# Kernel optimization log

Measured on AMD Instinct MI355X. Metric: run time of the kernel, lower is better.

The kernel has to match this reference:

```python
import jax, jax.numpy as jnp
import numpy as np

V, E, H, L = 100000, 128, 512, 9
B, T = 64, 512


def setup_inputs() -> dict:
    key = jax.random.key(0)
    ks = jax.random.split(key, 8)
    text = jax.random.randint(ks[0], (B, T), 0, V, dtype=jnp.int32)
    labels = jax.random.randint(ks[1], (B, T), 0, L, dtype=jnp.int32)
    embed = jax.random.normal(ks[2], (V, E), jnp.float32) * 0.02
    Wx = jax.random.normal(ks[3], (E, 4 * H), jnp.float32) * (1.0 / np.sqrt(E))
    Wh = jax.random.normal(ks[4], (H, 4 * H), jnp.float32) * (1.0 / np.sqrt(H))
    # Keras LSTM default: zero bias with unit forget-gate bias (gate order i,f,c,o)
    b = jnp.zeros((4 * H,), jnp.float32).at[H:2 * H].set(1.0)
    Wd = jax.random.normal(ks[5], (H, L), jnp.float32) * (1.0 / np.sqrt(H))
    bd = jnp.zeros((L,), jnp.float32)
    trans = jax.random.uniform(ks[6], (L, L), jnp.float32)
    return dict(text=text, labels=labels, embed=embed, Wx=Wx, Wh=Wh, b=b,
                Wd=Wd, bd=bd, trans=trans)


def _lstm(x, Wx, Wh, b):
    # x: [B,T,E] -> h: [B,T,H]; Keras gate order i,f,c,o
    Bx, Tx, _ = x.shape
    Hh = Wh.shape[0]
    xg = jnp.einsum('bte,eg->btg', x, Wx) + b  # precompute input projections [B,T,4H]

    def step(carry, g_t):
        h, c = carry
        g = g_t + h @ Wh
        i, f, cg, o = jnp.split(g, 4, axis=-1)
        c = jax.nn.sigmoid(f) * c + jax.nn.sigmoid(i) * jnp.tanh(cg)
        h = jax.nn.sigmoid(o) * jnp.tanh(c)
        return (h, c), h

    init = (jnp.zeros((Bx, Hh), x.dtype), jnp.zeros((Bx, Hh), x.dtype))
    _, hs = jax.lax.scan(step, init, jnp.moveaxis(xg, 1, 0))
    return jnp.moveaxis(hs, 0, 1)


def _crf_log_likelihood(logits, labels, lens, trans):
    # tfa.text.crf_log_likelihood: score(seq) - log_norm (forward algorithm)
    Bl, Tl, Ll = logits.shape
    t_idx = jnp.arange(Tl)
    mask = t_idx[None, :] < lens[:, None]  # [B,T]
    unary = jnp.take_along_axis(logits, labels[..., None], axis=2)[..., 0]
    unary = jnp.where(mask, unary, 0.0).sum(-1)
    binary = trans[labels[:, :-1], labels[:, 1:]]
    bmask = t_idx[1:][None, :] < lens[:, None]  # transition t->t+1 counts iff t+1 < len
    binary = jnp.where(bmask, binary, 0.0).sum(-1)
    score = unary + binary

    def step(alpha, xs):
        lg, t = xs  # lg: [B,L]
        new = jax.scipy.special.logsumexp(alpha[:, :, None] + trans[None], axis=1) + lg
        alpha = jnp.where((t < lens)[:, None], new, alpha)
        return alpha, None

    alpha0 = logits[:, 0]
    xs = (jnp.moveaxis(logits[:, 1:], 1, 0), jnp.arange(1, Tl))
    alpha, _ = jax.lax.scan(step, alpha0, xs)
    log_norm = jax.scipy.special.logsumexp(alpha, axis=-1)
    return score - log_norm


def reference(text, labels, embed, Wx, Wh, b, Wd, bd, trans):
    lens = jnp.sum((text != 0).astype(jnp.int32), axis=-1)
    x = embed[text]                      # [B,T,E] (dropout inactive at inference)
    h = _lstm(x, Wx, Wh, b)              # [B,T,H]
    logits = h @ Wd + bd                 # [B,T,L]
    ll = _crf_log_likelihood(logits, labels, lens, trans)  # [B]
    return logits, lens, ll
```

## Files before the change

kernel.cpp:

```cpp
#include <hip/hip_runtime.h>
#include <hip/hip_bf16.h>

#define V_SZ 100000
#define E_SZ 128
#define H_SZ 512
#define L_SZ 9
#define B_SZ 64
#define T_SZ 512
#define G4   (4*H_SZ)

#define LOGITS_N (B_SZ*T_SZ*L_SZ)
#define HS_BYTES ((size_t)B_SZ*T_SZ*H_SZ*2)

typedef short bf16x8 __attribute__((ext_vector_type(8)));
typedef float f32x4  __attribute__((ext_vector_type(4)));

static __device__ __forceinline__ unsigned short f2bf(float x){
  unsigned int u = __builtin_bit_cast(unsigned int, x);
  unsigned int r = (u + 0x7fffu + ((u >> 16) & 1u)) >> 16;
  return (unsigned short)r;
}
static __device__ __forceinline__ float bf2f(unsigned short b){
  unsigned int u = ((unsigned int)b) << 16;
  return __builtin_bit_cast(float, u);
}
static __device__ __forceinline__ float sig_f(float x){
  return 1.f / (1.f + __expf(-x));
}
static __device__ __forceinline__ float tanh_f(float x){
  float a = fabsf(x);
  float e = __expf(-2.f * a);
  float t = (1.f - e) / (1.f + e);
  return copysignf(t, x);
}

__global__ void k_lens(const int* __restrict__ text, float* __restrict__ out_lens){
  int b = blockIdx.x;
  int c = 0;
  for (int t = threadIdx.x; t < T_SZ; t += 256)
    c += (text[b*T_SZ + t] != 0);
  for (int off = 32; off; off >>= 1) c += __shfl_down(c, off, 64);
  __shared__ int sred[4];
  int w = threadIdx.x >> 6;
  if ((threadIdx.x & 63) == 0) sred[w] = c;
  __syncthreads();
  if (threadIdx.x == 0)
    out_lens[b] = (float)(sred[0] + sred[1] + sred[2] + sred[3]);
}

__global__ __launch_bounds__(256, 1)
void k_lstm(const int* __restrict__ text, const float* __restrict__ embed,
            const float* __restrict__ Wx, const float* __restrict__ Wh,
            const float* __restrict__ bias, unsigned short* __restrict__ hs,
            int* __restrict__ flags)
{
  const int g    = blockIdx.x & 7;
  const int j    = blockIdx.x >> 3;
  const int n0   = j * 16;
  const int tid  = threadIdx.x;
  const int w    = tid >> 6;
  const int lane = tid & 63;
  const int q    = lane >> 4;
  const int l16  = lane & 15;

  __shared__ unsigned short h_lds[16*512];
  __shared__ unsigned short x_lds[16*128];
  __shared__ float gate_lds[4][8][16];

  for (int i = tid; i < 16*512; i += 256) h_lds[i] = 0;
  for (int i = tid; i < 16*128; i += 256) x_lds[i] = 0;

  const int gcol = w * H_SZ + n0 + l16;
  bf16x8 Whf[16];
#pragma unroll
  for (int kk = 0; kk < 16; ++kk){
    bf16x8 v;
#pragma unroll
    for (int jj = 0; jj < 8; ++jj)
      v[jj] = (short)f2bf(Wh[(long)(kk*32 + q*8 + jj)*G4 + gcol]);
    Whf[kk] = v;
  }
  bf16x8 Wxf[4];
#pragma unroll
  for (int kk = 0; kk < 4; ++kk){
    bf16x8 v;
#pragma unroll
    for (int jj = 0; jj < 8; ++jj)
      v[jj] = (short)f2bf(Wx[(long)(kk*32 + q*8 + jj)*G4 + gcol]);
    Wxf[kk] = v;
  }
  const float biasv = bias[gcol];

  float cs0 = 0.f, cs1 = 0.f;
  const int gr = tid >> 3;
  const int gc2 = (tid & 7) * 2;

  __syncthreads();

  for (int t = 0; t < T_SZ; ++t){
    {
      int xr = tid >> 5;
      int c4 = (tid & 31) * 4;
      int idx = text[(g*8 + xr)*T_SZ + t];
      const float4 xv = *(const float4*)(embed + (long)idx*E_SZ + c4);
      int cb = c4 * 2;
      unsigned short* p = (unsigned short*)((char*)x_lds + xr*256 + (cb ^ (xr << 4)));
      p[0] = f2bf(xv.x); p[1] = f2bf(xv.y); p[2] = f2bf(xv.z); p[3] = f2bf(xv.w);
    }

    if (t > 0){
      if (tid < 64){
        const int* fl = flags + (g*T_SZ + (t-1))*32;
        int it = 0;
        for (;;){
          int f = 1;
          if (lane < 32)
            f = __hip_atomic_load(&fl[lane], __ATOMIC_RELAXED, __HIP_MEMORY_SCOPE_AGENT);
          if (__all(f != 0)) break;
          if (++it > (1 << 20)) break;
        }
      }
      __syncthreads();

#pragma unroll
      for (int c = 0; c < 4; ++c){
        int chunk = tid + 256*c;
        int hr    = chunk >> 7;
        int k4    = chunk & 127;
        unsigned long long v = __hip_atomic_load(
            (const unsigned long long*)(hs + ((long)(g*8 + hr)*T_SZ + (t-1))*H_SZ + k4*4),
            __ATOMIC_RELAXED, __HIP_MEMORY_SCOPE_AGENT);
        int cb = k4 * 8;
        *(unsigned long long*)((char*)h_lds + hr*1024 + (cb ^ (hr << 4))) = v;
      }
    }
    __syncthreads();

    f32x4 acc0 = {0.f,0.f,0.f,0.f}, acc1 = {0.f,0.f,0.f,0.f};
#pragma unroll
    for (int kk = 0; kk < 4; ++kk){
      bf16x8 a = *(const bf16x8*)((const char*)x_lds + l16*256 + ((kk*64 + q*16) ^ (l16 << 4)));
      if (kk & 1) acc1 = __builtin_amdgcn_mfma_f32_16x16x32_bf16(a, Wxf[kk], acc1, 0, 0, 0);
      else        acc0 = __builtin_amdgcn_mfma_f32_16x16x32_bf16(a, Wxf[kk], acc0, 0, 0, 0);
    }
    if (t > 0){
#pragma unroll
      for (int kk = 0; kk < 16; ++kk){
        bf16x8 a = *(const bf16x8*)((const char*)h_lds + l16*1024 + ((kk*64 + q*16) ^ (l16 << 4)));
        if (kk & 1) acc1 = __builtin_amdgcn_mfma_f32_16x16x32_bf16(a, Whf[kk], acc1, 0, 0, 0);
        else        acc0 = __builtin_amdgcn_mfma_f32_16x16x32_bf16(a, Whf[kk], acc0, 0, 0, 0);
      }
    }
#pragma unroll
    for (int rg = 0; rg < 4; ++rg){
      int row = q*4 + rg;
      if (row < 8) gate_lds[w][row][l16] = acc0[rg] + acc1[rg] + biasv;
    }
    __syncthreads();

    if (tid < 64){
      float gi0 = gate_lds[0][gr][gc2],   gi1 = gate_lds[0][gr][gc2+1];
      float gf0 = gate_lds[1][gr][gc2],   gf1 = gate_lds[1][gr][gc2+1];
      float gg0 = gate_lds[2][gr][gc2],   gg1 = gate_lds[2][gr][gc2+1];
      float go0 = gate_lds[3][gr][gc2],   go1 = gate_lds[3][gr][gc2+1];
      cs0 = sig_f(gf0)*cs0 + sig_f(gi0)*tanh_f(gg0);
      cs1 = sig_f(gf1)*cs1 + sig_f(gi1)*tanh_f(gg1);
      float h0 = sig_f(go0)*tanh_f(cs0);
      float h1 = sig_f(go1)*tanh_f(cs1);
      unsigned int pk = (unsigned int)f2bf(h0) | ((unsigned int)f2bf(h1) << 16);
      __hip_atomic_store(
          (unsigned int*)(hs + ((long)(g*8 + gr)*T_SZ + t)*H_SZ + n0 + gc2), pk,
          __ATOMIC_RELAXED, __HIP_MEMORY_SCOPE_AGENT);
      asm volatile("s_waitcnt vmcnt(0)" ::: "memory");
      if (tid == 0)
        __hip_atomic_store(&flags[(g*T_SZ + t)*32 + j], 1,
                           __ATOMIC_RELAXED, __HIP_MEMORY_SCOPE_AGENT);
    }
  }
}

__global__ void k_logits(const unsigned short* __restrict__ hs,
                         const float* __restrict__ Wd, const float* __restrict__ bd,
                         float* __restrict__ out)
{
  __shared__ float wd_s[H_SZ*L_SZ];
  __shared__ float bd_s[L_SZ];
  for (int i = threadIdx.x; i < H_SZ*L_SZ; i += 128) wd_s[i] = Wd[i];
  if (threadIdx.x < L_SZ) bd_s[threadIdx.x] = bd[threadIdx.x];
  __syncthreads();

  long row = (long)blockIdx.x*128 + threadIdx.x;
  const unsigned short* hp = hs + row*H_SZ;
  float acc[9];
#pragma unroll
  for (int jj = 0; jj < 9; ++jj) acc[jj] = 0.f;
  for (int k = 0; k < H_SZ; k += 8){
    uint4 v = *(const uint4*)(hp + k);
    const unsigned short* u = (const unsigned short*)&v;
#pragma unroll
    for (int l = 0; l < 8; ++l){
      float hf = bf2f(u[l]);
#pragma unroll
      for (int jj = 0; jj < 9; ++jj)
        acc[jj] = fmaf(hf, wd_s[(k + l)*L_SZ + jj], acc[jj]);
    }
  }
  float* op = out + row*L_SZ;
#pragma unroll
  for (int jj = 0; jj < 9; ++jj) op[jj] = acc[jj] + bd_s[jj];
}

__global__ void k_crf(const float* __restrict__ logits, const int* __restrict__ labels,
                      const float* __restrict__ trans, const float* __restrict__ lensf,
                      float* __restrict__ out_ll)
{
  int b = blockIdx.x;
  int lane = threadIdx.x;
  int len = (int)lensf[b];
  const float* lg  = logits + (long)b*T_SZ*L_SZ;
  const int*   lab = labels + b*T_SZ;

  float s = 0.f;
  for (int t = lane; t < T_SZ; t += 64){
    if (t < len){
      s += lg[t*L_SZ + lab[t]];
      if (t >= 1) s += trans[lab[t-1]*L_SZ + lab[t]];
    }
  }
  for (int off = 32; off; off >>= 1) s += __shfl_down(s, off, 64);

  float tr[9];
#pragma unroll
  for (int i = 0; i < 9; ++i) tr[i] = (lane < 9) ? trans[i*L_SZ + lane] : 0.f;
  float alpha = (lane < 9) ? lg[lane] : -1e30f;

  for (int t = 1; t < T_SZ; ++t){
    float tmp[9];
    float m = -1e30f;
#pragma unroll
    for (int i = 0; i < 9; ++i){
      float ai = __shfl(alpha, i, 64);
      tmp[i] = ai + tr[i];
      m = fmaxf(m, tmp[i]);
    }
    float e = 0.f;
#pragma unroll
    for (int i = 0; i < 9; ++i) e += __expf(tmp[i] - m);
    float lgv = (lane < 9) ? lg[t*L_SZ + lane] : 0.f;
    float nv = m + __logf(e) + lgv;
    if (t < len && lane < 9) alpha = nv;
  }

  float mm = (lane < 9) ? alpha : -1e30f;
  for (int off = 8; off; off >>= 1) mm = fmaxf(mm, __shfl_down(mm, off, 64));
  mm = __shfl(mm, 0, 64);
  float ee = (lane < 9) ? __expf(alpha - mm) : 0.f;
  for (int off = 8; off; off >>= 1) ee += __shfl_down(ee, off, 64);
  if (lane == 0) out_ll[b] = s - (mm + __logf(ee));
}

extern "C" void kernel_launch(void* const* d_in, const int* in_sizes, int n_in,
                              void* d_out, int out_size, void* d_ws, size_t ws_size,
                              hipStream_t stream)
{
  const int*   text   = (const int*)  d_in[0];
  const int*   labels = (const int*)  d_in[1];
  const float* embed  = (const float*)d_in[2];
  const float* Wx     = (const float*)d_in[3];
  const float* Wh     = (const float*)d_in[4];
  const float* bias   = (const float*)d_in[5];
  const float* Wd     = (const float*)d_in[6];
  const float* bd     = (const float*)d_in[7];
  const float* trans  = (const float*)d_in[8];

  float* out        = (float*)d_out;
  float* out_logits = out;
  float* out_lens   = out + LOGITS_N;
  float* out_ll     = out + LOGITS_N + B_SZ;

  unsigned short* hs = (unsigned short*)d_ws;
  int* flags = (int*)((char*)d_ws + HS_BYTES);

  hipMemsetAsync(flags, 0, 8*T_SZ*32*sizeof(int), stream);
  k_lens  <<<B_SZ, 256, 0, stream>>>(text, out_lens);
  k_lstm  <<<256, 256, 0, stream>>>(text, embed, Wx, Wh, bias, hs, flags);
  k_logits<<<256, 128, 0, stream>>>(hs, Wd, bd, out_logits);
  k_crf   <<<B_SZ, 64, 0, stream>>>(out_logits, labels, trans, out_lens, out_ll);
}
```

Measured before the change: 1.731 ms.

## Replace flag-based LSTM sync with sentinel polling and interleave two batch groups per block

The hidden-state buffer is pre-filled with a NaN sentinel so consumer blocks poll the h data directly instead of separate per-step flags. This removes the flag writes, the vmcnt wait and one barrier from each step. Each block now handles two batch groups in alternation, halving the grid to 128 blocks so one group's latency can hide behind the other's work. It adds a full 32MB sentinel reset pass, and a real bf16 value equal to the sentinel pattern would cause a spin until timeout. The CRF max reduction is also restructured into a tree.

```diff
diff --git a/kernel.cpp b/kernel.cpp
--- a/kernel.cpp
+++ b/kernel.cpp
@@ -11,6 +11,8 @@
 
 #define LOGITS_N (B_SZ*T_SZ*L_SZ)
 #define HS_BYTES ((size_t)B_SZ*T_SZ*H_SZ*2)
+#define SENT32 0x7FC07FC0u
+#define SENT64 0x7FC07FC07FC07FC0ull
 
 typedef short bf16x8 __attribute__((ext_vector_type(8)));
 typedef float f32x4  __attribute__((ext_vector_type(4)));
@@ -32,6 +34,12 @@
   float e = __expf(-2.f * a);
   float t = (1.f - e) / (1.f + e);
   return copysignf(t, x);
+}
+
+__global__ void k_reset(unsigned long long* __restrict__ hs64){
+  const long n = HS_BYTES / 8;
+  for (long i = (long)blockIdx.x*256 + threadIdx.x; i < n; i += (long)gridDim.x*256)
+    __hip_atomic_store(&hs64[i], SENT64, __ATOMIC_RELAXED, __HIP_MEMORY_SCOPE_AGENT);
 }
 
 __global__ void k_lens(const int* __restrict__ text, float* __restrict__ out_lens){
@@ -51,11 +59,11 @@
 __global__ __launch_bounds__(256, 1)
 void k_lstm(const int* __restrict__ text, const float* __restrict__ embed,
             const float* __restrict__ Wx, const float* __restrict__ Wh,
-            const float* __restrict__ bias, unsigned short* __restrict__ hs,
-            int* __restrict__ flags)
+            const float* __restrict__ bias, unsigned short* __restrict__ hs)
 {
-  const int g    = blockIdx.x & 7;
-  const int j    = blockIdx.x >> 3;
+  const int p    = blockIdx.x & 3;
+  const int j    = blockIdx.x >> 2;
+  const int gA   = 2*p, gB = 2*p + 1;
   const int n0   = j * 16;
   const int tid  = threadIdx.x;
   const int w    = tid >> 6;
@@ -91,47 +99,48 @@
   }
   const float biasv = bias[gcol];
 
-  float cs0 = 0.f, cs1 = 0.f;
-  const int gr = tid >> 3;
+  float csA0 = 0.f, csA1 = 0.f, csB0 = 0.f, csB1 = 0.f;
+  const int gr  = tid >> 3;
   const int gc2 = (tid & 7) * 2;
 
+  const int k4     = tid & 127;
+  const int hrbase = tid >> 7;
+
   __syncthreads();
 
-  for (int t = 0; t < T_SZ; ++t){
+  auto phase = [&](int g, int t, float& cs0, float& cs1){
     {
       int xr = tid >> 5;
       int c4 = (tid & 31) * 4;
       int idx = text[(g*8 + xr)*T_SZ + t];
       const float4 xv = *(const float4*)(embed + (long)idx*E_SZ + c4);
       int cb = c4 * 2;
-      unsigned short* p = (unsigned short*)((char*)x_lds + xr*256 + (cb ^ (xr << 4)));
-      p[0] = f2bf(xv.x); p[1] = f2bf(xv.y); p[2] = f2bf(xv.z); p[3] = f2bf(xv.w);
+      unsigned short* pp = (unsigned short*)((char*)x_lds + xr*256 + (cb ^ (xr << 4)));
+      pp[0] = f2bf(xv.x); pp[1] = f2bf(xv.y); pp[2] = f2bf(xv.z); pp[3] = f2bf(xv.w);
     }
 
     if (t > 0){
-      if (tid < 64){
-        const int* fl = flags + (g*T_SZ + (t-1))*32;
-        int it = 0;
-        for (;;){
-          int f = 1;
-          if (lane < 32)
-            f = __hip_atomic_load(&fl[lane], __ATOMIC_RELAXED, __HIP_MEMORY_SCOPE_AGENT);
-          if (__all(f != 0)) break;
-          if (++it > (1 << 20)) break;
+      unsigned long long v[4];
+      int it = 0; bool ok;
+      do {
+        ok = true;
+#pragma unroll
+        for (int c = 0; c < 4; ++c){
+          int hrow = hrbase + 2*c;
+          v[c] = __hip_atomic_load(
+              (const unsigned long long*)(hs + ((long)(g*8 + hrow)*T_SZ + (t-1))*H_SZ + k4*4),
+              __ATOMIC_RELAXED, __HIP_MEMORY_SCOPE_AGENT);
         }
-      }
-      __syncthreads();
-
+#pragma unroll
+        for (int c = 0; c < 4; ++c){
+          unsigned int lo = (unsigned int)v[c], hi = (unsigned int)(v[c] >> 32);
+          ok = ok && (lo != SENT32) && (hi != SENT32);
+        }
+      } while (!ok && ++it < (1 << 20));
 #pragma unroll
       for (int c = 0; c < 4; ++c){
-        int chunk = tid + 256*c;
-        int hr    = chunk >> 7;
-        int k4    = chunk & 127;
-        unsigned long long v = __hip_atomic_load(
-            (const unsigned long long*)(hs + ((long)(g*8 + hr)*T_SZ + (t-1))*H_SZ + k4*4),
-            __ATOMIC_RELAXED, __HIP_MEMORY_SCOPE_AGENT);
-        int cb = k4 * 8;
-        *(unsigned long long*)((char*)h_lds + hr*1024 + (cb ^ (hr << 4))) = v;
+        int hrow = hrbase + 2*c;
+        *(unsigned long long*)((char*)h_lds + hrow*1024 + ((k4*8) ^ (hrow << 4))) = v[c];
       }
     }
     __syncthreads();
@@ -159,10 +168,10 @@
     __syncthreads();
 
     if (tid < 64){
-      float gi0 = gate_lds[0][gr][gc2],   gi1 = gate_lds[0][gr][gc2+1];
-      float gf0 = gate_lds[1][gr][gc2],   gf1 = gate_lds[1][gr][gc2+1];
-      float gg0 = gate_lds[2][gr][gc2],   gg1 = gate_lds[2][gr][gc2+1];
-      float go0 = gate_lds[3][gr][gc2],   go1 = gate_lds[3][gr][gc2+1];
+      float gi0 = gate_lds[0][gr][gc2], gi1 = gate_lds[0][gr][gc2+1];
+      float gf0 = gate_lds[1][gr][gc2], gf1 = gate_lds[1][gr][gc2+1];
+      float gg0 = gate_lds[2][gr][gc2], gg1 = gate_lds[2][gr][gc2+1];
+      float go0 = gate_lds[3][gr][gc2], go1 = gate_lds[3][gr][gc2+1];
       cs0 = sig_f(gf0)*cs0 + sig_f(gi0)*tanh_f(gg0);
       cs1 = sig_f(gf1)*cs1 + sig_f(gi1)*tanh_f(gg1);
       float h0 = sig_f(go0)*tanh_f(cs0);
@@ -171,11 +180,12 @@
       __hip_atomic_store(
           (unsigned int*)(hs + ((long)(g*8 + gr)*T_SZ + t)*H_SZ + n0 + gc2), pk,
           __ATOMIC_RELAXED, __HIP_MEMORY_SCOPE_AGENT);
-      asm volatile("s_waitcnt vmcnt(0)" ::: "memory");
-      if (tid == 0)
-        __hip_atomic_store(&flags[(g*T_SZ + t)*32 + j], 1,
-                           __ATOMIC_RELAXED, __HIP_MEMORY_SCOPE_AGENT);
-    }
+    }
+  };
+
+  for (int t = 0; t < T_SZ; ++t){
+    phase(gA, t, csA0, csA1);
+    phase(gB, t, csB0, csB1);
   }
 }
 
@@ -236,13 +246,15 @@
 
   for (int t = 1; t < T_SZ; ++t){
     float tmp[9];
-    float m = -1e30f;
 #pragma unroll
     for (int i = 0; i < 9; ++i){
       float ai = __shfl(alpha, i, 64);
       tmp[i] = ai + tr[i];
-      m = fmaxf(m, tmp[i]);
-    }
+    }
+    float m0 = fmaxf(fmaxf(tmp[0], tmp[1]), tmp[2]);
+    float m1 = fmaxf(fmaxf(tmp[3], tmp[4]), tmp[5]);
+    float m2 = fmaxf(fmaxf(tmp[6], tmp[7]), tmp[8]);
+    float m  = fmaxf(fmaxf(m0, m1), m2);
     float e = 0.f;
 #pragma unroll
     for (int i = 0; i < 9; ++i) e += __expf(tmp[i] - m);
@@ -279,11 +291,10 @@
   float* out_ll     = out + LOGITS_N + B_SZ;
 
   unsigned short* hs = (unsigned short*)d_ws;
-  int* flags = (int*)((char*)d_ws + HS_BYTES);
-
-  hipMemsetAsync(flags, 0, 8*T_SZ*32*sizeof(int), stream);
+
+  k_reset <<<2048, 256, 0, stream>>>((unsigned long long*)hs);
   k_lens  <<<B_SZ, 256, 0, stream>>>(text, out_lens);
-  k_lstm  <<<256, 256, 0, stream>>>(text, embed, Wx, Wh, bias, hs, flags);
+  k_lstm  <<<128, 256, 0, stream>>>(text, embed, Wx, Wh, bias, hs);
   k_logits<<<256, 128, 0, stream>>>(hs, Wd, bd, out_logits);
   k_crf   <<<B_SZ, 64, 0, stream>>>(out_logits, labels, trans, out_lens, out_ll);
 }
```

New measurement: 2.015 ms. +16.4%, slower.
